# Kernel optimization log

Hardware: AMD Instinct MI355X
Metric: run time of the kernel (lower is better)

The kernel has to match this reference:

```python
import jax, jax.numpy as jnp
import numpy as np

N_EMBD = 768
N_HEAD = 12
B, T = 4, 2048
EPS = 1e-5


def layernorm(x, w, b):
    mu = jnp.mean(x, axis=-1, keepdims=True)
    var = jnp.mean(jnp.square(x - mu), axis=-1, keepdims=True)
    return (x - mu) * jax.lax.rsqrt(var + EPS) * w + b


def setup_inputs() -> dict:
    key = jax.random.key(0)
    ks = jax.random.split(key, 6)
    C = N_EMBD
    s = 0.02
    return {
        "x": jax.random.normal(ks[0], (B, T, C), jnp.float32),
        "ln1_w": jnp.ones((C,), jnp.float32),
        "ln1_b": jnp.zeros((C,), jnp.float32),
        "W_qkv": jax.random.normal(ks[1], (C, 3 * C), jnp.float32) * s,
        "b_qkv": jnp.zeros((3 * C,), jnp.float32),
        "W_attnproj": jax.random.normal(ks[2], (C, C), jnp.float32) * s,
        "b_attnproj": jnp.zeros((C,), jnp.float32),
        "ln2_w": jnp.ones((C,), jnp.float32),
        "ln2_b": jnp.zeros((C,), jnp.float32),
        "W_fc": jax.random.normal(ks[3], (C, 4 * C), jnp.float32) * s,
        "b_fc": jnp.zeros((4 * C,), jnp.float32),
        "W_mlpproj": jax.random.normal(ks[4], (4 * C, C), jnp.float32) * s,
        "b_mlpproj": jnp.zeros((C,), jnp.float32),
    }


def reference(x, ln1_w, ln1_b, W_qkv, b_qkv, W_attnproj, b_attnproj,
              ln2_w, ln2_b, W_fc, b_fc, W_mlpproj, b_mlpproj):
    Bx, Tx, C = x.shape
    H = N_HEAD
    Dh = C // H

    # --- attention branch ---
    h = layernorm(x, ln1_w, ln1_b)
    qkv = h @ W_qkv + b_qkv                       # [B, T, 3C]
    q, k, v = jnp.split(qkv, 3, axis=-1)
    q = q.reshape(Bx, Tx, H, Dh).transpose(0, 2, 1, 3)  # [B, H, T, Dh]
    k = k.reshape(Bx, Tx, H, Dh).transpose(0, 2, 1, 3)
    v = v.reshape(Bx, Tx, H, Dh).transpose(0, 2, 1, 3)
    att = jnp.einsum('bhqd,bhkd->bhqk', q, k) * (1.0 / np.sqrt(Dh))
    att = jax.nn.softmax(att, axis=-1)            # full softmax attention (no mask)
    y = jnp.einsum('bhqk,bhkd->bhqd', att, v)     # [B, H, T, Dh]
    y = y.transpose(0, 2, 1, 3).reshape(Bx, Tx, C)
    y = y @ W_attnproj + b_attnproj
    x = x + y

    # --- MLP branch ---
    h = layernorm(x, ln2_w, ln2_b)
    h = jax.nn.gelu(h @ W_fc + b_fc, approximate=False)
    h = h @ W_mlpproj + b_mlpproj
    return x + h
```

## Files before the change

### kernel.cpp

```cpp
#include <hip/hip_runtime.h>

typedef __bf16 bf16x8 __attribute__((ext_vector_type(8)));
typedef __bf16 bf16x4 __attribute__((ext_vector_type(4)));
typedef float f32x4 __attribute__((ext_vector_type(4)));
typedef unsigned short u16;
typedef unsigned long long u64;

#define GL2LDS(gp, lp) __builtin_amdgcn_global_load_lds(                      \
    (const __attribute__((address_space(1))) void*)(gp),                      \
    (__attribute__((address_space(3))) void*)(lp), 16, 0, 0)

__device__ __forceinline__ u16 f2u(float f) {
    __bf16 h = (__bf16)f;
    return __builtin_bit_cast(u16, h);
}

__device__ __forceinline__ float fexp2(float x) {
    float r;
    asm("v_exp_f32 %0, %1" : "=v"(r) : "v"(x));
    return r;
}

__device__ __forceinline__ float frcp(float x) {
    float r;
    asm("v_rcp_f32 %0, %1" : "=v"(r) : "v"(x));
    return r;
}

__device__ __forceinline__ float gelu(float x) {
    const float a = x * x;
    const float b = fmaf(a, 0.10294323f, 2.30220795f);
    const float u = fexp2(x * b);
    const float r = frcp(1.0f + u);
    return (x > 8.0f) ? x : x * u * r;
}

template <int N>
__device__ __forceinline__ void waitv() {
    if constexpr (N == 0) asm volatile("s_waitcnt vmcnt(0)" ::: "memory");
    else if constexpr (N == 4) asm volatile("s_waitcnt vmcnt(4)" ::: "memory");
    else if constexpr (N == 5) asm volatile("s_waitcnt vmcnt(5)" ::: "memory");
    else if constexpr (N == 6) asm volatile("s_waitcnt vmcnt(6)" ::: "memory");
}

__device__ __forceinline__ f32x4 mfma16(bf16x8 a, bf16x8 b, f32x4 c) {
    return __builtin_amdgcn_mfma_f32_16x16x32_bf16(a, b, c, 0, 0, 0);
}

__global__ __launch_bounds__(256) void transpose_kernel(
    const float* __restrict__ W, u16* __restrict__ Wt, int K, int N) {
    __shared__ float tile[32][33];
    const int tx = threadIdx.x & 31, ty = threadIdx.x >> 5;
    const int n0 = blockIdx.x * 32, k0 = blockIdx.y * 32;
#pragma unroll
    for (int i = 0; i < 4; i++)
        tile[ty + 8 * i][tx] = W[(size_t)(k0 + ty + 8 * i) * N + n0 + tx];
    __syncthreads();
#pragma unroll
    for (int i = 0; i < 4; i++)
        Wt[(size_t)(n0 + ty + 8 * i) * K + k0 + tx] = f2u(tile[tx][ty + 8 * i]);
}

__global__ __launch_bounds__(256) void ln_kernel(
    const float* __restrict__ xin, const float* __restrict__ wgt,
    const float* __restrict__ bia, u16* __restrict__ outp) {
    const int row = blockIdx.x, t = threadIdx.x;
    const float* xr = xin + (size_t)row * 768;
    float v0 = xr[t], v1 = xr[t + 256], v2 = xr[t + 512];
    float s = v0 + v1 + v2;
    float ss = v0 * v0 + v1 * v1 + v2 * v2;
#pragma unroll
    for (int off = 32; off; off >>= 1) {
        s += __shfl_xor(s, off);
        ss += __shfl_xor(ss, off);
    }
    __shared__ float red[8];
    const int w = t >> 6;
    if ((t & 63) == 0) { red[w] = s; red[4 + w] = ss; }
    __syncthreads();
    s  = red[0] + red[1] + red[2] + red[3];
    ss = red[4] + red[5] + red[6] + red[7];
    const float mu = s * (1.f / 768.f);
    const float var = ss * (1.f / 768.f) - mu * mu;
    const float rs = rsqrtf(var + 1e-5f);
    u16* orow = outp + (size_t)row * 768;
    orow[t]       = f2u((v0 - mu) * rs * wgt[t]       + bia[t]);
    orow[t + 256] = f2u((v1 - mu) * rs * wgt[t + 256] + bia[t + 256]);
    orow[t + 512] = f2u((v2 - mu) * rs * wgt[t + 512] + bia[t + 512]);
}

template <int EPI>
__global__ __launch_bounds__(256, 3) void gemm96(
    const u16* __restrict__ A, const u16* __restrict__ Bt,
    const float* __restrict__ bias, void* __restrict__ outp,
    u16* __restrict__ vt, int M, int N, int K) {
    __shared__ __align__(16) u16 As[2][4096];
    __shared__ __align__(16) u16 Bs[2][6144];
    const int t = threadIdx.x;
    const int lane = t & 63, w = t >> 6;
    const int wg0 = blockIdx.y * gridDim.x + blockIdx.x;
    const int xcd = wg0 & 7, loc = wg0 >> 3;
    const int gx = gridDim.x, gy = gridDim.y;
    const int m0 = (xcd * (gy >> 3) + loc / gx) * 128;
    const int n0 = (loc % gx) * 192;
    const int wm = (w >> 1) * 64, wn = (w & 1) * 96;
    const int lq = lane & 15, g = lane >> 4;

    f32x4 acc[4][6];
#pragma unroll
    for (int i = 0; i < 4; i++)
#pragma unroll
        for (int j = 0; j < 6; j++) acc[i][j] = (f32x4){0.f, 0.f, 0.f, 0.f};

    const int srow = t >> 2;
    const int scol = ((t & 3) ^ ((t >> 3) & 3)) * 8;
    const u16* gA0 = A + (size_t)(m0 + srow) * K + scol;
    const u16* gA1 = A + (size_t)(m0 + 64 + srow) * K + scol;
    const u16* gB0 = Bt + (size_t)(n0 + srow) * K + scol;
    const u16* gB1 = Bt + (size_t)(n0 + 64 + srow) * K + scol;
    const u16* gB2 = Bt + (size_t)(n0 + 128 + srow) * K + scol;

    const int cph = (g ^ ((lq >> 1) & 3)) << 4;
    const int KT = K >> 5;

#define STAGE96(buf, kt)                                                      \
    do {                                                                      \
        const int ko_ = (kt) << 5;                                            \
        GL2LDS(gA0 + ko_, (char*)As[buf] + w * 1024);                         \
        GL2LDS(gA1 + ko_, (char*)As[buf] + 4096 + w * 1024);                  \
        GL2LDS(gB0 + ko_, (char*)Bs[buf] + w * 1024);                         \
        GL2LDS(gB1 + ko_, (char*)Bs[buf] + 4096 + w * 1024);                  \
        GL2LDS(gB2 + ko_, (char*)Bs[buf] + 8192 + w * 1024);                  \
    } while (0)

    STAGE96(0, 0);
    STAGE96(1, 1);
    for (int kt = 0; kt < KT; ++kt) {
        if (kt + 1 < KT) waitv<5>(); else waitv<0>();
        __builtin_amdgcn_s_barrier();
        __builtin_amdgcn_sched_barrier(0);
        const char* rA = (char*)As[kt & 1] + (wm + lq) * 64 + cph;
        const char* rB = (char*)Bs[kt & 1] + (wn + lq) * 64 + cph;
        bf16x8 af[4];
#pragma unroll
        for (int m = 0; m < 4; m++) af[m] = *(const bf16x8*)(rA + m * 1024);
        __builtin_amdgcn_s_setprio(1);
#pragma unroll
        for (int n = 0; n < 6; n++) {
            const bf16x8 bfr = *(const bf16x8*)(rB + n * 1024);
#pragma unroll
            for (int m = 0; m < 4; m++)
                acc[m][n] = mfma16(af[m], bfr, acc[m][n]);
        }
        __builtin_amdgcn_s_setprio(0);
        __builtin_amdgcn_sched_barrier(0);
        __builtin_amdgcn_s_barrier();
        if (kt + 2 < KT) STAGE96(kt & 1, kt + 2);
    }
#undef STAGE96

#pragma unroll
    for (int n = 0; n < 6; n++) {
        const int col = n0 + wn + 16 * n + lq;
        const float bv = bias[col];
#pragma unroll
        for (int m = 0; m < 4; m++) {
            const int rbase = m0 + wm + 16 * m + 4 * g;
            if constexpr (EPI == 0) {
                if (col < 1536) {
                    const float qs = (col < 768) ? 0.18033688f : 1.0f;
#pragma unroll
                    for (int r = 0; r < 4; r++) {
                        const size_t idx = (size_t)(rbase + r) * N + col;
                        ((u16*)outp)[idx] = f2u((acc[m][n][r] + bv) * qs);
                    }
                } else {
                    const int d = col - 1536;
                    bf16x4 pk;
#pragma unroll
                    for (int r = 0; r < 4; r++)
                        pk[r] = (__bf16)(acc[m][n][r] + bv);
                    u16* vrow = vt +
                        ((size_t)((rbase >> 11) * 12 + (d >> 6)) * 64 + (d & 63)) * 2048 +
                        (rbase & 2047);
                    *(u64*)vrow = __builtin_bit_cast(u64, pk);
                }
            } else {
#pragma unroll
                for (int r = 0; r < 4; r++) {
                    const size_t idx = (size_t)(rbase + r) * N + col;
                    ((u16*)outp)[idx] = f2u(gelu(acc[m][n][r] + bv));
                }
            }
        }
    }
}

__global__ __launch_bounds__(256, 3) void gemm_k64(
    const u16* __restrict__ A, const u16* __restrict__ Bt,
    const float* __restrict__ bias, const float* __restrict__ res,
    float* __restrict__ outp, int M, int N, int K) {
    __shared__ __align__(16) u16 As[2][4096];
    __shared__ __align__(16) u16 Bs[2][8192];
    const int t = threadIdx.x;
    const int lane = t & 63, w = t >> 6;
    const int wg0 = blockIdx.y * gridDim.x + blockIdx.x;
    const int xcd = wg0 & 7, loc = wg0 >> 3;
    const int gx = gridDim.x, gy = gridDim.y;
    const int m0 = (xcd * (gy >> 3) + loc / gx) * 64;
    const int n0 = (loc % gx) * 128;
    const int wm = (w >> 1) * 32, wn = (w & 1) * 64;
    const int lq = lane & 15, g = lane >> 4;

    f32x4 acc[2][4];
#pragma unroll
    for (int i = 0; i < 2; i++)
#pragma unroll
        for (int j = 0; j < 4; j++) acc[i][j] = (f32x4){0.f, 0.f, 0.f, 0.f};

    const int srow8 = w * 8 + (lane >> 3);
    const int scol = ((lane & 7) ^ (lane >> 3)) * 8;
    const u16* gA_0 = A + (size_t)(m0 + srow8) * K + scol;
    const u16* gA_1 = A + (size_t)(m0 + 32 + srow8) * K + scol;
    const u16* gB_0 = Bt + (size_t)(n0 + srow8) * K + scol;
    const u16* gB_1 = Bt + (size_t)(n0 + 32 + srow8) * K + scol;
    const u16* gB_2 = Bt + (size_t)(n0 + 64 + srow8) * K + scol;
    const u16* gB_3 = Bt + (size_t)(n0 + 96 + srow8) * K + scol;

    const int KT = K >> 6;

#define STAGE64(buf, kt)                                                      \
    do {                                                                      \
        const int ko_ = (kt) << 6;                                            \
        GL2LDS(gA_0 + ko_, (char*)As[buf] + w * 1024);                        \
        GL2LDS(gA_1 + ko_, (char*)As[buf] + 4096 + w * 1024);                 \
        GL2LDS(gB_0 + ko_, (char*)Bs[buf] + w * 1024);                        \
        GL2LDS(gB_1 + ko_, (char*)Bs[buf] + 4096 + w * 1024);                 \
        GL2LDS(gB_2 + ko_, (char*)Bs[buf] + 8192 + w * 1024);                 \
        GL2LDS(gB_3 + ko_, (char*)Bs[buf] + 12288 + w * 1024);                \
    } while (0)

    STAGE64(0, 0);
    STAGE64(1, 1);
    for (int kt = 0; kt < KT; ++kt) {
        if (kt + 1 < KT) waitv<6>(); else waitv<0>();
        __builtin_amdgcn_s_barrier();
        __builtin_amdgcn_sched_barrier(0);
        const char* aB = (char*)As[kt & 1] + (wm + lq) * 128;
        const char* bB = (char*)Bs[kt & 1] + (wn + lq) * 128;
        const int sw = lq & 7;
#pragma unroll
        for (int s = 0; s < 2; s++) {
            const int co = (((s << 2) + g) ^ sw) << 4;
            bf16x8 af[2], bfr[4];
#pragma unroll
            for (int m = 0; m < 2; m++)
                af[m] = *(const bf16x8*)(aB + m * 2048 + co);
#pragma unroll
            for (int n = 0; n < 4; n++)
                bfr[n] = *(const bf16x8*)(bB + n * 2048 + co);
            __builtin_amdgcn_s_setprio(1);
#pragma unroll
            for (int m = 0; m < 2; m++)
#pragma unroll
                for (int n = 0; n < 4; n++)
                    acc[m][n] = mfma16(af[m], bfr[n], acc[m][n]);
            __builtin_amdgcn_s_setprio(0);
        }
        __builtin_amdgcn_sched_barrier(0);
        __builtin_amdgcn_s_barrier();
        if (kt + 2 < KT) STAGE64(kt & 1, kt + 2);
    }
#undef STAGE64

#pragma unroll
    for (int n = 0; n < 4; n++) {
        const int col = n0 + wn + 16 * n + lq;
        const float bv = bias[col];
#pragma unroll
        for (int m = 0; m < 2; m++) {
            const int rbase = m0 + wm + 16 * m + 4 * g;
#pragma unroll
            for (int r = 0; r < 4; r++) {
                const size_t idx = (size_t)(rbase + r) * N + col;
                outp[idx] = acc[m][n][r] + bv + res[idx];
            }
        }
    }
}

__global__ __launch_bounds__(256, 3) void attn_kernel(
    const u16* __restrict__ qkv, const u16* __restrict__ Vt,
    u16* __restrict__ y) {
    __shared__ __align__(16) u16 Ks[2][4096];
    __shared__ __align__(16) u16 Vts[2][4096];
    __shared__ __align__(16) u16 Ps[4][2048];
    const int t = threadIdx.x, lane = t & 63, w = t >> 6;
    int wg = blockIdx.y * gridDim.x + blockIdx.x;
    wg = (wg & 7) * ((gridDim.x * gridDim.y) >> 3) + (wg >> 3);
    const int bh = wg / gridDim.x;
    const int b = bh / 12, h = bh % 12;
    const int q0 = (wg % gridDim.x) * 128 + w * 32;
    const int lq = lane & 15, g = lane >> 4;
    const int swz = (lq & 7) << 4;

    bf16x8 qf[2][2];
#pragma unroll
    for (int qh = 0; qh < 2; qh++) {
        const u16* qp =
            qkv + (size_t)(b * 2048 + q0 + qh * 16 + lq) * 2304 + h * 64 + g * 8;
        qf[qh][0] = *(const bf16x8*)(qp);
        qf[qh][1] = *(const bf16x8*)(qp + 32);
    }
    bf16x8 ones;
#pragma unroll
    for (int i = 0; i < 8; i++) ones[i] = (__bf16)1.0f;

    f32x4 acc_o[2][4], acc_s[2];
#pragma unroll
    for (int qh = 0; qh < 2; qh++) {
        acc_s[qh] = (f32x4){0.f, 0.f, 0.f, 0.f};
#pragma unroll
        for (int f = 0; f < 4; f++) acc_o[qh][f] = (f32x4){0.f, 0.f, 0.f, 0.f};
    }

    const int srow = t >> 3, sc = (t & 7) ^ (srow & 7);
    const u16* kg = qkv + 768 + h * 64 + sc * 8 + (size_t)(b * 2048 + srow) * 2304;
    const u16* vg = Vt + (size_t)(bh * 64 + srow) * 2048 + sc * 8;

#define STAGEKV(buf, kt)                                                      \
    do {                                                                      \
        const int kn_ = (kt) * 64;                                            \
        GL2LDS(kg + (size_t)kn_ * 2304, (char*)Ks[buf] + w * 1024);           \
        GL2LDS(kg + (size_t)(kn_ + 32) * 2304,                                \
               (char*)Ks[buf] + w * 1024 + 4096);                             \
        GL2LDS(vg + kn_, (char*)Vts[buf] + w * 1024);                         \
        GL2LDS(vg + 32 * 2048 + kn_, (char*)Vts[buf] + w * 1024 + 4096);      \
    } while (0)

    STAGEKV(0, 0);
    STAGEKV(1, 1);
    for (int kt = 0; kt < 32; ++kt) {
        const int buf = kt & 1;
        if (kt + 1 < 32) waitv<4>(); else waitv<0>();
        __builtin_amdgcn_s_barrier();
        __builtin_amdgcn_sched_barrier(0);
        const char* KB = (const char*)Ks[buf];
        const char* VB = (const char*)Vts[buf];

        f32x4 st[2][4];
        __builtin_amdgcn_s_setprio(1);
#pragma unroll
        for (int kb = 0; kb < 4; kb++) {
            st[0][kb] = (f32x4){0.f, 0.f, 0.f, 0.f};
            st[1][kb] = (f32x4){0.f, 0.f, 0.f, 0.f};
            const char* kr = KB + (kb * 16 + lq) * 128;
#pragma unroll
            for (int dh = 0; dh < 2; dh++) {
                const bf16x8 kf =
                    *(const bf16x8*)(kr + ((((dh << 2) + g) << 4) ^ swz));
                st[0][kb] = mfma16(kf, qf[0][dh], st[0][kb]);
                st[1][kb] = mfma16(kf, qf[1][dh], st[1][kb]);
            }
        }
        __builtin_amdgcn_s_setprio(0);

#pragma unroll
        for (int qh = 0; qh < 2; qh++) {
            char* pw = (char*)Ps[w] + (qh * 16 + lq) * 128 + ((g & 1) << 3);
#pragma unroll
            for (int kb = 0; kb < 4; kb++) {
                bf16x4 pb;
#pragma unroll
                for (int r = 0; r < 4; r++)
                    pb[r] = (__bf16)fexp2(st[qh][kb][r]);
                *(u64*)(pw + ((((kb << 1) + (g >> 1)) << 4) ^ swz)) =
                    __builtin_bit_cast(u64, pb);
            }
        }

        __builtin_amdgcn_s_setprio(1);
#pragma unroll
        for (int kk = 0; kk < 2; kk++) {
            const int co = ((kk << 2) + g) << 4;
            bf16x8 vf[4];
#pragma unroll
            for (int f = 0; f < 4; f++)
                vf[f] = *(const bf16x8*)(VB + (16 * f + lq) * 128 + (co ^ swz));
#pragma unroll
            for (int qh = 0; qh < 2; qh++) {
                const bf16x8 pf = *(const bf16x8*)(
                    (const char*)Ps[w] + (qh * 16 + lq) * 128 + (co ^ swz));
#pragma unroll
                for (int f = 0; f < 4; f++)
                    acc_o[qh][f] = mfma16(vf[f], pf, acc_o[qh][f]);
                acc_s[qh] = mfma16(ones, pf, acc_s[qh]);
            }
        }
        __builtin_amdgcn_s_setprio(0);
        __builtin_amdgcn_sched_barrier(0);
        __builtin_amdgcn_s_barrier();
        if (kt + 2 < 32) STAGEKV(buf, kt + 2);
    }
#undef STAGEKV

#pragma unroll
    for (int qh = 0; qh < 2; qh++) {
        const float rinv = frcp(acc_s[qh][0]);
        char* yb = (char*)(y + (size_t)(b * 2048 + q0 + qh * 16 + lq) * 768 +
                           h * 64);
#pragma unroll
        for (int f = 0; f < 4; f++) {
            bf16x4 pk;
#pragma unroll
            for (int r = 0; r < 4; r++) pk[r] = (__bf16)(acc_o[qh][f][r] * rinv);
            *(u64*)(yb + f * 32 + g * 8) = __builtin_bit_cast(u64, pk);
        }
    }
}

extern "C" void kernel_launch(void* const* d_in, const int* in_sizes, int n_in,
                              void* d_out, int out_size, void* d_ws,
                              size_t ws_size, hipStream_t stream) {
    const float* x    = (const float*)d_in[0];
    const float* ln1w = (const float*)d_in[1];
    const float* ln1b = (const float*)d_in[2];
    const float* Wqkv = (const float*)d_in[3];
    const float* bqkv = (const float*)d_in[4];
    const float* Wap  = (const float*)d_in[5];
    const float* bap  = (const float*)d_in[6];
    const float* ln2w = (const float*)d_in[7];
    const float* ln2b = (const float*)d_in[8];
    const float* Wfc  = (const float*)d_in[9];
    const float* bfc  = (const float*)d_in[10];
    const float* Wmp  = (const float*)d_in[11];
    const float* bmp  = (const float*)d_in[12];
    float* out = (float*)d_out;

    char* ws = (char*)d_ws;
    u16* Wt_qkv = (u16*)(ws);
    u16* Wt_ap  = (u16*)(ws + 3538944);
    u16* Wt_fc  = (u16*)(ws + 4718592);
    u16* Wt_mp  = (u16*)(ws + 9437184);
    u16* bufA   = (u16*)(ws + 14155776);
    u16* bufB   = (u16*)(ws + 26738688);
    u16* VtBuf  = (u16*)(ws + 64487424);

    transpose_kernel<<<dim3(72, 24), 256, 0, stream>>>(Wqkv, Wt_qkv, 768, 2304);
    transpose_kernel<<<dim3(24, 24), 256, 0, stream>>>(Wap, Wt_ap, 768, 768);
    transpose_kernel<<<dim3(96, 24), 256, 0, stream>>>(Wfc, Wt_fc, 768, 3072);
    transpose_kernel<<<dim3(24, 96), 256, 0, stream>>>(Wmp, Wt_mp, 3072, 768);

    ln_kernel<<<8192, 256, 0, stream>>>(x, ln1w, ln1b, bufA);
    gemm96<0><<<dim3(12, 64), 256, 0, stream>>>(
        bufA, Wt_qkv, bqkv, bufB, VtBuf, 8192, 2304, 768);
    attn_kernel<<<dim3(16, 48), 256, 0, stream>>>(bufB, VtBuf, bufA);
    gemm_k64<<<dim3(6, 128), 256, 0, stream>>>(
        bufA, Wt_ap, bap, x, out, 8192, 768, 768);
    ln_kernel<<<8192, 256, 0, stream>>>(out, ln2w, ln2b, bufA);
    gemm96<2><<<dim3(16, 64), 256, 0, stream>>>(
        bufA, Wt_fc, bfc, bufB, nullptr, 8192, 3072, 768);
    gemm_k64<<<dim3(6, 128), 256, 0, stream>>>(
        bufB, Wt_mp, bmp, out, out, 8192, 768, 3072);
}
```

Before: 261.6 us.

## Replace double-buffered 64-key attention tiles with single-buffered 128-key tiles

The attention kernel drops its double-buffered 64-key K/V pipeline. It now loads one 128-key K/V tile per iteration into a single buffer, waits for all loads, and processes the tile in two halves. This halves the number of barrier and wait rounds. It also removes overlap between global-to-LDS loads and compute, so load latency is exposed on every iteration.

```diff
diff --git a/kernel.cpp b/kernel.cpp
--- a/kernel.cpp
+++ b/kernel.cpp
@@ -292,8 +292,8 @@
 __global__ __launch_bounds__(256, 3) void attn_kernel(
     const u16* __restrict__ qkv, const u16* __restrict__ Vt,
     u16* __restrict__ y) {
-    __shared__ __align__(16) u16 Ks[2][4096];
-    __shared__ __align__(16) u16 Vts[2][4096];
+    __shared__ __align__(16) u16 Ks[8192];
+    __shared__ __align__(16) u16 Vts[8192];
     __shared__ __align__(16) u16 Ps[4][2048];
     const int t = threadIdx.x, lane = t & 63, w = t >> 6;
     int wg = blockIdx.y * gridDim.x + blockIdx.x;
@@ -326,83 +326,81 @@
 
     const int srow = t >> 3, sc = (t & 7) ^ (srow & 7);
     const u16* kg = qkv + 768 + h * 64 + sc * 8 + (size_t)(b * 2048 + srow) * 2304;
-    const u16* vg = Vt + (size_t)(bh * 64 + srow) * 2048 + sc * 8;
-
-#define STAGEKV(buf, kt)                                                      \
-    do {                                                                      \
-        const int kn_ = (kt) * 64;                                            \
-        GL2LDS(kg + (size_t)kn_ * 2304, (char*)Ks[buf] + w * 1024);           \
-        GL2LDS(kg + (size_t)(kn_ + 32) * 2304,                                \
-               (char*)Ks[buf] + w * 1024 + 4096);                             \
-        GL2LDS(vg + kn_, (char*)Vts[buf] + w * 1024);                         \
-        GL2LDS(vg + 32 * 2048 + kn_, (char*)Vts[buf] + w * 1024 + 4096);      \
-    } while (0)
-
-    STAGEKV(0, 0);
-    STAGEKV(1, 1);
-    for (int kt = 0; kt < 32; ++kt) {
-        const int buf = kt & 1;
-        if (kt + 1 < 32) waitv<4>(); else waitv<0>();
-        __builtin_amdgcn_s_barrier();
-        __builtin_amdgcn_sched_barrier(0);
-        const char* KB = (const char*)Ks[buf];
-        const char* VB = (const char*)Vts[buf];
-
-        f32x4 st[2][4];
-        __builtin_amdgcn_s_setprio(1);
-#pragma unroll
-        for (int kb = 0; kb < 4; kb++) {
-            st[0][kb] = (f32x4){0.f, 0.f, 0.f, 0.f};
-            st[1][kb] = (f32x4){0.f, 0.f, 0.f, 0.f};
-            const char* kr = KB + (kb * 16 + lq) * 128;
-#pragma unroll
-            for (int dh = 0; dh < 2; dh++) {
-                const bf16x8 kf =
-                    *(const bf16x8*)(kr + ((((dh << 2) + g) << 4) ^ swz));
-                st[0][kb] = mfma16(kf, qf[0][dh], st[0][kb]);
-                st[1][kb] = mfma16(kf, qf[1][dh], st[1][kb]);
+    const int vrow = t >> 4, vc = (t & 15) ^ (vrow & 7);
+    const u16* vg = Vt + (size_t)(bh * 64 + vrow) * 2048 + vc * 8;
+
+    for (int kt = 0; kt < 16; ++kt) {
+        const int k0 = kt * 128;
+#pragma unroll
+        for (int i = 0; i < 4; i++)
+            GL2LDS(kg + (size_t)(k0 + 32 * i) * 2304,
+                   (char*)Ks + i * 4096 + w * 1024);
+#pragma unroll
+        for (int j = 0; j < 4; j++)
+            GL2LDS(vg + k0 + j * 32768, (char*)Vts + j * 4096 + w * 1024);
+        waitv<0>();
+        __builtin_amdgcn_s_barrier();
+        __builtin_amdgcn_sched_barrier(0);
+
+#pragma unroll
+        for (int half = 0; half < 2; half++) {
+            const char* KB = (const char*)Ks + half * 64 * 128;
+            f32x4 st[2][4];
+            __builtin_amdgcn_s_setprio(1);
+#pragma unroll
+            for (int kb = 0; kb < 4; kb++) {
+                st[0][kb] = (f32x4){0.f, 0.f, 0.f, 0.f};
+                st[1][kb] = (f32x4){0.f, 0.f, 0.f, 0.f};
+                const char* kr = KB + (kb * 16 + lq) * 128;
+#pragma unroll
+                for (int dh = 0; dh < 2; dh++) {
+                    const bf16x8 kf =
+                        *(const bf16x8*)(kr + ((((dh << 2) + g) << 4) ^ swz));
+                    st[0][kb] = mfma16(kf, qf[0][dh], st[0][kb]);
+                    st[1][kb] = mfma16(kf, qf[1][dh], st[1][kb]);
+                }
             }
-        }
-        __builtin_amdgcn_s_setprio(0);
-
-#pragma unroll
-        for (int qh = 0; qh < 2; qh++) {
-            char* pw = (char*)Ps[w] + (qh * 16 + lq) * 128 + ((g & 1) << 3);
-#pragma unroll
-            for (int kb = 0; kb < 4; kb++) {
-                bf16x4 pb;
-#pragma unroll
-                for (int r = 0; r < 4; r++)
-                    pb[r] = (__bf16)fexp2(st[qh][kb][r]);
-                *(u64*)(pw + ((((kb << 1) + (g >> 1)) << 4) ^ swz)) =
-                    __builtin_bit_cast(u64, pb);
+            __builtin_amdgcn_s_setprio(0);
+
+#pragma unroll
+            for (int qh = 0; qh < 2; qh++) {
+                char* pw = (char*)Ps[w] + (qh * 16 + lq) * 128 + ((g & 1) << 3);
+#pragma unroll
+                for (int kb = 0; kb < 4; kb++) {
+                    bf16x4 pb;
+#pragma unroll
+                    for (int r = 0; r < 4; r++)
+                        pb[r] = (__bf16)fexp2(st[qh][kb][r]);
+                    *(u64*)(pw + ((((kb << 1) + (g >> 1)) << 4) ^ swz)) =
+                        __builtin_bit_cast(u64, pb);
+                }
             }
-        }
-
-        __builtin_amdgcn_s_setprio(1);
-#pragma unroll
-        for (int kk = 0; kk < 2; kk++) {
-            const int co = ((kk << 2) + g) << 4;
-            bf16x8 vf[4];
-#pragma unroll
-            for (int f = 0; f < 4; f++)
-                vf[f] = *(const bf16x8*)(VB + (16 * f + lq) * 128 + (co ^ swz));
-#pragma unroll
-            for (int qh = 0; qh < 2; qh++) {
-                const bf16x8 pf = *(const bf16x8*)(
-                    (const char*)Ps[w] + (qh * 16 + lq) * 128 + (co ^ swz));
+
+            __builtin_amdgcn_s_setprio(1);
+#pragma unroll
+            for (int kk = 0; kk < 2; kk++) {
+                bf16x8 vf[4];
 #pragma unroll
                 for (int f = 0; f < 4; f++)
-                    acc_o[qh][f] = mfma16(vf[f], pf, acc_o[qh][f]);
-                acc_s[qh] = mfma16(ones, pf, acc_s[qh]);
+                    vf[f] = *(const bf16x8*)(
+                        (const char*)Vts + (16 * f + lq) * 256 +
+                        ((((half << 3) + (kk << 2) + g) ^ (lq & 7)) << 4));
+                const int co = ((kk << 2) + g) << 4;
+#pragma unroll
+                for (int qh = 0; qh < 2; qh++) {
+                    const bf16x8 pf = *(const bf16x8*)(
+                        (const char*)Ps[w] + (qh * 16 + lq) * 128 + (co ^ swz));
+#pragma unroll
+                    for (int f = 0; f < 4; f++)
+                        acc_o[qh][f] = mfma16(vf[f], pf, acc_o[qh][f]);
+                    acc_s[qh] = mfma16(ones, pf, acc_s[qh]);
+                }
             }
-        }
-        __builtin_amdgcn_s_setprio(0);
-        __builtin_amdgcn_sched_barrier(0);
-        __builtin_amdgcn_s_barrier();
-        if (kt + 2 < 32) STAGEKV(buf, kt + 2);
-    }
-#undef STAGEKV
+            __builtin_amdgcn_s_setprio(0);
+        }
+        __builtin_amdgcn_sched_barrier(0);
+        __builtin_amdgcn_s_barrier();
+    }
 
 #pragma unroll
     for (int qh = 0; qh < 2; qh++) {
```

Result: no change. 262.7 us (+0.4%).
